# Kernel optimization log

Hardware: AMD Instinct MI355X
Metric: run time of the kernel (lower is better)

The kernel has to match this reference:

```python
import jax, jax.numpy as jnp
import numpy as np

N_LAYERS = 3


def setup_inputs() -> dict:
    key = jax.random.key(0)
    k1, k2, k3, k4 = jax.random.split(key, 4)
    n_users, n_items, d, E = 600000, 400000, 64, 2000000
    return {
        "user_emb": jax.random.normal(k1, (n_users, d), dtype=jnp.float32) * 0.1,
        "item_emb": jax.random.normal(k2, (n_items, d), dtype=jnp.float32) * 0.1,
        "user_ids": jax.random.randint(k3, (E,), 0, n_users, dtype=jnp.int64),
        "item_ids": jax.random.randint(k4, (E,), 0, n_items, dtype=jnp.int64),
    }


def reference(user_emb, item_emb, user_ids, item_ids):
    n_users = user_emb.shape[0]
    n_items = item_emb.shape[0]
    n_nodes = n_users + n_items
    # symmetrized bipartite edge list (user->item and item->user)
    rows = jnp.concatenate([user_ids, item_ids + n_users])
    cols = jnp.concatenate([item_ids + n_users, user_ids])
    # degree = row-sum of binary adjacency (duplicates counted, matching csr sum)
    deg = jax.ops.segment_sum(jnp.ones(rows.shape, dtype=user_emb.dtype), rows,
                              num_segments=n_nodes)
    d_inv_sqrt = (deg + 1e-8) ** -0.5
    vals = d_inv_sqrt[rows] * d_inv_sqrt[cols]  # per-edge normalized weight

    emb = jnp.concatenate([user_emb, item_emb], axis=0)  # [n_nodes, d]
    acc = emb
    x = emb
    for _ in range(N_LAYERS):
        x = jax.ops.segment_sum(vals[:, None] * x[cols], rows, num_segments=n_nodes)
        acc = acc + x
    final = acc / (N_LAYERS + 1)  # mean over stacked layer outputs
    return final[:n_users], final[n_users:]
```

## Files before the change

### kernel.cpp

```cpp
#include <hip/hip_runtime.h>


#define BLK 256
#define SCAN_CHUNK 2048
#define FILL_EPB 2048

typedef unsigned int u32;
typedef unsigned char u8;
typedef float __attribute__((ext_vector_type(4))) f32x4;

static inline int nblk(long long total) { return (int)((total + BLK - 1) / BLK); }

__device__ inline u32 pack_bf2(float lo, float hi) {
    u32 a = __float_as_uint(lo);
    u32 b = __float_as_uint(hi);
    a = a + 0x7fffu + ((a >> 16) & 1u);
    b = b + 0x7fffu + ((b >> 16) & 1u);
    return (a >> 16) | (b & 0xffff0000u);
}

__device__ inline void unpack_acc(uint4 w, float* a) {
    a[0] += __uint_as_float(w.x << 16);
    a[1] += __uint_as_float(w.x & 0xffff0000u);
    a[2] += __uint_as_float(w.y << 16);
    a[3] += __uint_as_float(w.y & 0xffff0000u);
    a[4] += __uint_as_float(w.z << 16);
    a[5] += __uint_as_float(w.z & 0xffff0000u);
    a[6] += __uint_as_float(w.w << 16);
    a[7] += __uint_as_float(w.w & 0xffff0000u);
}

__device__ inline void unpack8(uint4 w, float* a) {
    a[0] = __uint_as_float(w.x << 16);
    a[1] = __uint_as_float(w.x & 0xffff0000u);
    a[2] = __uint_as_float(w.y << 16);
    a[3] = __uint_as_float(w.y & 0xffff0000u);
    a[4] = __uint_as_float(w.z << 16);
    a[5] = __uint_as_float(w.z & 0xffff0000u);
    a[6] = __uint_as_float(w.w << 16);
    a[7] = __uint_as_float(w.w & 0xffff0000u);
}

__global__ void deg_rank_kernel(const int* __restrict__ uid,
                                const int* __restrict__ iid,
                                int E, int n_users,
                                u32* __restrict__ degw,
                                u32* __restrict__ rank2) {
    int t = blockIdx.x * blockDim.x + threadIdx.x;
    if (t < E) {
        u32 u  = (u32)uid[t];
        u32 iN = (u32)(n_users + iid[t]);
        u32 su = 8u * (u & 3u), si = 8u * (iN & 3u);
        u32 r0 = atomicAdd(&degw[u >> 2],  1u << su);
        u32 r1 = atomicAdd(&degw[iN >> 2], 1u << si);
        r0 = (r0 >> su) & 0xffu;
        r1 = (r1 >> si) & 0xffu;
        rank2[t] = r0 | (r1 << 16);
    }
}

__global__ void dinv_kernel(const u8* __restrict__ deg8,
                            float* __restrict__ dinv, int n_nodes) {
    int t = blockIdx.x * blockDim.x + threadIdx.x;
    if (t < n_nodes) dinv[t] = rsqrtf((float)deg8[t] + 1e-8f);
}

__global__ void scan1_kernel(const u8* __restrict__ deg8,
                             u32* __restrict__ rp, u32* __restrict__ bsum, int n) {
    __shared__ u32 ts[256];
    int tid = threadIdx.x;
    int base = blockIdx.x * SCAN_CHUNK + tid * 8;
    u32 v[8];
    u32 s = 0;
    #pragma unroll
    for (int i = 0; i < 8; ++i) {
        v[i] = (base + i < n) ? (u32)deg8[base + i] : 0u;
        s += v[i];
    }
    ts[tid] = s;
    __syncthreads();
    for (int off = 1; off < 256; off <<= 1) {
        u32 a = (tid >= off) ? ts[tid - off] : 0u;
        __syncthreads();
        ts[tid] += a;
        __syncthreads();
    }
    u32 run = (tid > 0) ? ts[tid - 1] : 0u;
    #pragma unroll
    for (int i = 0; i < 8; ++i) {
        run += v[i];
        if (base + i < n) rp[base + i + 1] = run;
    }
    if (tid == 255) bsum[blockIdx.x] = ts[255];
}

__global__ void scan2_kernel(u32* __restrict__ bsum, int nb) {
    __shared__ u32 s[1024];
    int tid = threadIdx.x;
    s[tid] = (tid < nb) ? bsum[tid] : 0u;
    __syncthreads();
    for (int off = 1; off < 1024; off <<= 1) {
        u32 a = (tid >= off) ? s[tid - off] : 0u;
        __syncthreads();
        s[tid] += a;
        __syncthreads();
    }
    if (tid < nb) bsum[tid] = (tid == 0) ? 0u : s[tid - 1];
}

__global__ void scan3_kernel(u32* __restrict__ rp,
                             const u32* __restrict__ bsum, int n) {
    int t = blockIdx.x * blockDim.x + threadIdx.x;
    if (t < n) rp[t + 1] += bsum[t / SCAN_CHUNK];
    if (t == 0) rp[0] = 0u;
}

__global__ void fill_sliced_kernel(const int* __restrict__ uid,
                                   const int* __restrict__ iid,
                                   const u32* __restrict__ rank2,
                                   const u32* __restrict__ rp,
                                   int E, int n_users, int shift,
                                   int* __restrict__ ci) {
    int slice = blockIdx.x & 7;
    int chunk = blockIdx.x >> 3;
    int e0   = chunk * FILL_EPB;
    int eend = min(E, e0 + FILL_EPB);
    for (int e = e0 + threadIdx.x; e < eend; e += BLK) {
        int u  = uid[e];
        int iN = n_users + iid[e];
        u32 rr = rank2[e];
        if ((u >> shift) == slice)  ci[rp[u]  + (rr & 0xffffu)] = iN;
        if ((iN >> shift) == slice) ci[rp[iN] + (rr >> 16)]     = u;
    }
}

__global__ void z0_full_kernel(const f32x4* __restrict__ uemb,
                               const f32x4* __restrict__ iemb,
                               const float* __restrict__ dinv,
                               uint4* __restrict__ z0,
                               int n_users, int n_nodes) {
    long long t = (long long)blockIdx.x * blockDim.x + threadIdx.x;
    if (t >= (long long)n_nodes * 8) return;
    int row = (int)(t >> 3);
    int j   = (int)(t & 7);
    const f32x4* src = (row < n_users)
                           ? uemb + (size_t)row * 16 + j * 2
                           : iemb + (size_t)(row - n_users) * 16 + j * 2;
    f32x4 p = __builtin_nontemporal_load(src);
    f32x4 q = __builtin_nontemporal_load(src + 1);
    float w = dinv[row];
    uint4 o;
    o.x = pack_bf2(w * p.x, w * p.y);
    o.y = pack_bf2(w * p.z, w * p.w);
    o.z = pack_bf2(w * q.x, w * q.y);
    o.w = pack_bf2(w * q.z, w * q.w);
    z0[(size_t)row * 8 + j] = o;
}

__global__ void spmm_mid64(const u32* __restrict__ rp,
                           const int* __restrict__ ci,
                           const float* __restrict__ dinv,
                           const uint4* __restrict__ src,
                           uint4* __restrict__ dst, int n_nodes) {
    long long t = (long long)blockIdx.x * blockDim.x + threadIdx.x;
    int row = (int)(t >> 3);
    if (row >= n_nodes) return;
    int j = (int)(t & 7);
    const uint4* sp = src + j;
    u32 k = rp[row], end = rp[row + 1];
    float a[8] = {0.f, 0.f, 0.f, 0.f, 0.f, 0.f, 0.f, 0.f};
    for (; k + 3 < end; k += 4) {
        int c0 = ci[k], c1 = ci[k + 1], c2 = ci[k + 2], c3 = ci[k + 3];
        uint4 w0 = sp[(size_t)c0 * 8];
        uint4 w1 = sp[(size_t)c1 * 8];
        uint4 w2 = sp[(size_t)c2 * 8];
        uint4 w3 = sp[(size_t)c3 * 8];
        unpack_acc(w0, a); unpack_acc(w1, a);
        unpack_acc(w2, a); unpack_acc(w3, a);
    }
    for (; k < end; ++k) {
        uint4 w0 = sp[(size_t)ci[k] * 8];
        unpack_acc(w0, a);
    }
    float dr = dinv[row];
    float s = dr * dr;
    uint4 o;
    o.x = pack_bf2(s * a[0], s * a[1]);
    o.y = pack_bf2(s * a[2], s * a[3]);
    o.z = pack_bf2(s * a[4], s * a[5]);
    o.w = pack_bf2(s * a[6], s * a[7]);
    dst[(size_t)row * 8 + j] = o;
}

__global__ void spmm_final64(const u32* __restrict__ rp,
                             const int* __restrict__ ci,
                             const float* __restrict__ dinv,
                             const uint4* __restrict__ z2,
                             const uint4* __restrict__ z1,
                             const uint4* __restrict__ z0,
                             f32x4* __restrict__ out, int n_nodes) {
    long long t = (long long)blockIdx.x * blockDim.x + threadIdx.x;
    int row = (int)(t >> 3);
    if (row >= n_nodes) return;
    int j = (int)(t & 7);
    const uint4* sp = z2 + j;
    u32 k = rp[row], end = rp[row + 1];
    float a[8] = {0.f, 0.f, 0.f, 0.f, 0.f, 0.f, 0.f, 0.f};
    for (; k + 3 < end; k += 4) {
        int c0 = ci[k], c1 = ci[k + 1], c2 = ci[k + 2], c3 = ci[k + 3];
        uint4 w0 = sp[(size_t)c0 * 8];
        uint4 w1 = sp[(size_t)c1 * 8];
        uint4 w2 = sp[(size_t)c2 * 8];
        uint4 w3 = sp[(size_t)c3 * 8];
        unpack_acc(w0, a); unpack_acc(w1, a);
        unpack_acc(w2, a); unpack_acc(w3, a);
    }
    for (; k < end; ++k) {
        uint4 w0 = sp[(size_t)ci[k] * 8];
        unpack_acc(w0, a);
    }
    float dr = dinv[row];
    float inv = 1.0f / dr;

    float v0[8], v1[8], v2[8];
    unpack8(z0[(size_t)row * 8 + j], v0);
    unpack8(z1[(size_t)row * 8 + j], v1);
    unpack8(z2[(size_t)row * 8 + j], v2);

    float r[8];
    #pragma unroll
    for (int i = 0; i < 8; ++i)
        r[i] = 0.25f * ((v0[i] + v1[i] + v2[i]) * inv + dr * a[i]);

    size_t ob = (size_t)row * 16 + j * 2;
    f32x4 lo = {r[0], r[1], r[2], r[3]};
    f32x4 hi = {r[4], r[5], r[6], r[7]};
    __builtin_nontemporal_store(lo, out + ob);
    __builtin_nontemporal_store(hi, out + ob + 1);
}

extern "C" void kernel_launch(void* const* d_in, const int* in_sizes, int n_in,
                              void* d_out, int out_size, void* d_ws, size_t ws_size,
                              hipStream_t stream) {
    const float* uemb = (const float*)d_in[0];
    const float* iemb = (const float*)d_in[1];
    const int*   uid  = (const int*)d_in[2];
    const int*   iid  = (const int*)d_in[3];

    const int d = 64;
    int n_users = in_sizes[0] / d;
    int n_items = in_sizes[1] / d;
    int E       = in_sizes[2];
    int n_nodes = n_users + n_items;
    long long nnz = 2LL * E;

    auto align256 = [](size_t x) { return (x + 255) & ~(size_t)255; };
    size_t deg_b  = align256((size_t)n_nodes + 4);
    size_t rp_b   = align256((size_t)(n_nodes + 1) * 4);
    size_t dinv_b = align256((size_t)n_nodes * 4);
    size_t ci_b   = align256((size_t)nnz * 4);
    size_t rk_b   = align256((size_t)E * 4);
    size_t bs_b   = align256(4096 * 4);
    size_t z_b    = align256((size_t)n_nodes * 128);

    char* p = (char*)d_ws;
    u32*   degw  = (u32*)p;    p += deg_b;
    u32*   rp    = (u32*)p;    p += rp_b;
    float* dinv  = (float*)p;  p += dinv_b;
    int*   ci    = (int*)p;    p += ci_b;
    u32*   rank2 = (u32*)p;    p += rk_b;
    u32*   bsum  = (u32*)p;    p += bs_b;
    uint4* z0    = (uint4*)p;  p += z_b;
    uint4* z1    = (uint4*)p;  p += z_b;
    uint4* z2    = (uint4*)p;

    int shift = 0;
    while (((n_nodes - 1) >> shift) >= 8) shift++;

    hipMemsetAsync(degw, 0, (size_t)n_nodes + 4, stream);
    deg_rank_kernel<<<nblk(E), BLK, 0, stream>>>(uid, iid, E, n_users, degw, rank2);
    dinv_kernel<<<nblk(n_nodes), BLK, 0, stream>>>((const u8*)degw, dinv, n_nodes);

    int nb = (n_nodes + SCAN_CHUNK - 1) / SCAN_CHUNK;
    scan1_kernel<<<nb, 256, 0, stream>>>((const u8*)degw, rp, bsum, n_nodes);
    scan2_kernel<<<1, 1024, 0, stream>>>(bsum, nb);
    scan3_kernel<<<nblk(n_nodes), BLK, 0, stream>>>(rp, bsum, n_nodes);

    int nchunks = (E + FILL_EPB - 1) / FILL_EPB;
    fill_sliced_kernel<<<nchunks * 8, BLK, 0, stream>>>(
        uid, iid, rank2, rp, E, n_users, shift, ci);

    long long nt = (long long)n_nodes * 8;
    z0_full_kernel<<<nblk(nt), BLK, 0, stream>>>(
        (const f32x4*)uemb, (const f32x4*)iemb, dinv, z0, n_users, n_nodes);
    spmm_mid64<<<nblk(nt), BLK, 0, stream>>>(rp, ci, dinv, z0, z1, n_nodes);
    spmm_mid64<<<nblk(nt), BLK, 0, stream>>>(rp, ci, dinv, z1, z2, n_nodes);
    spmm_final64<<<nblk(nt), BLK, 0, stream>>>(rp, ci, dinv, z2, z1, z0,
                                               (f32x4*)d_out, n_nodes);
}
```

Measured before the change: 712.0 us.

## Fuse embedding bf16 conversion into degree kernel and scale by dinv in first SpMM

The bf16 conversion of the input embeddings no longer depends on the degree normalization. It now runs in the same launch as the degree/rank atomics, using a block-index split, so it can overlap with that atomic-bound work. The first SpMM instead gathers dinv per neighbor and applies the source-side scaling on the fly. The final combine is adjusted because z0 is now unscaled. This removes one dependent kernel launch from the critical path but adds per-edge dinv gathers in the first propagation layer.

```diff
diff --git a/kernel.cpp b/kernel.cpp
--- a/kernel.cpp
+++ b/kernel.cpp
@@ -30,6 +30,17 @@
     a[7] += __uint_as_float(w.w & 0xffff0000u);
 }
 
+__device__ inline void unpack_acc_s(uint4 w, float s, float* a) {
+    a[0] += s * __uint_as_float(w.x << 16);
+    a[1] += s * __uint_as_float(w.x & 0xffff0000u);
+    a[2] += s * __uint_as_float(w.y << 16);
+    a[3] += s * __uint_as_float(w.y & 0xffff0000u);
+    a[4] += s * __uint_as_float(w.z << 16);
+    a[5] += s * __uint_as_float(w.z & 0xffff0000u);
+    a[6] += s * __uint_as_float(w.w << 16);
+    a[7] += s * __uint_as_float(w.w & 0xffff0000u);
+}
+
 __device__ inline void unpack8(uint4 w, float* a) {
     a[0] = __uint_as_float(w.x << 16);
     a[1] = __uint_as_float(w.x & 0xffff0000u);
@@ -41,21 +52,41 @@
     a[7] = __uint_as_float(w.w & 0xffff0000u);
 }
 
-__global__ void deg_rank_kernel(const int* __restrict__ uid,
-                                const int* __restrict__ iid,
-                                int E, int n_users,
-                                u32* __restrict__ degw,
-                                u32* __restrict__ rank2) {
-    int t = blockIdx.x * blockDim.x + threadIdx.x;
-    if (t < E) {
-        u32 u  = (u32)uid[t];
-        u32 iN = (u32)(n_users + iid[t]);
-        u32 su = 8u * (u & 3u), si = 8u * (iN & 3u);
-        u32 r0 = atomicAdd(&degw[u >> 2],  1u << su);
-        u32 r1 = atomicAdd(&degw[iN >> 2], 1u << si);
-        r0 = (r0 >> su) & 0xffu;
-        r1 = (r1 >> si) & 0xffu;
-        rank2[t] = r0 | (r1 << 16);
+__global__ void fused_deg_conv(const int* __restrict__ uid,
+                               const int* __restrict__ iid,
+                               int E, int n_users,
+                               u32* __restrict__ degw,
+                               u32* __restrict__ rank2,
+                               const f32x4* __restrict__ uemb,
+                               const f32x4* __restrict__ iemb,
+                               uint4* __restrict__ z0,
+                               int n_nodes, int nblk_deg) {
+    if ((int)blockIdx.x < nblk_deg) {
+        int t = blockIdx.x * BLK + threadIdx.x;
+        if (t < E) {
+            u32 u  = (u32)uid[t];
+            u32 iN = (u32)(n_users + iid[t]);
+            u32 su = 8u * (u & 3u), si = 8u * (iN & 3u);
+            u32 r0 = atomicAdd(&degw[u >> 2],  1u << su);
+            u32 r1 = atomicAdd(&degw[iN >> 2], 1u << si);
+            rank2[t] = ((r0 >> su) & 0xffu) | (((r1 >> si) & 0xffu) << 16);
+        }
+    } else {
+        long long t = (long long)(blockIdx.x - nblk_deg) * BLK + threadIdx.x;
+        if (t >= (long long)n_nodes * 8) return;
+        int row = (int)(t >> 3);
+        int j   = (int)(t & 7);
+        const f32x4* src = (row < n_users)
+                               ? uemb + (size_t)row * 16 + j * 2
+                               : iemb + (size_t)(row - n_users) * 16 + j * 2;
+        f32x4 p = __builtin_nontemporal_load(src);
+        f32x4 q = __builtin_nontemporal_load(src + 1);
+        uint4 o;
+        o.x = pack_bf2(p.x, p.y);
+        o.y = pack_bf2(p.z, p.w);
+        o.z = pack_bf2(q.x, q.y);
+        o.w = pack_bf2(q.z, q.w);
+        z0[(size_t)row * 8 + j] = o;
     }
 }
 
@@ -134,27 +165,41 @@
     }
 }
 
-__global__ void z0_full_kernel(const f32x4* __restrict__ uemb,
-                               const f32x4* __restrict__ iemb,
-                               const float* __restrict__ dinv,
-                               uint4* __restrict__ z0,
-                               int n_users, int n_nodes) {
+__global__ void spmm_first64(const u32* __restrict__ rp,
+                             const int* __restrict__ ci,
+                             const float* __restrict__ dinv,
+                             const uint4* __restrict__ z0p,
+                             uint4* __restrict__ dst, int n_nodes) {
     long long t = (long long)blockIdx.x * blockDim.x + threadIdx.x;
-    if (t >= (long long)n_nodes * 8) return;
     int row = (int)(t >> 3);
-    int j   = (int)(t & 7);
-    const f32x4* src = (row < n_users)
-                           ? uemb + (size_t)row * 16 + j * 2
-                           : iemb + (size_t)(row - n_users) * 16 + j * 2;
-    f32x4 p = __builtin_nontemporal_load(src);
-    f32x4 q = __builtin_nontemporal_load(src + 1);
-    float w = dinv[row];
+    if (row >= n_nodes) return;
+    int j = (int)(t & 7);
+    const uint4* sp = z0p + j;
+    u32 k = rp[row], end = rp[row + 1];
+    float a[8] = {0.f, 0.f, 0.f, 0.f, 0.f, 0.f, 0.f, 0.f};
+    for (; k + 3 < end; k += 4) {
+        int c0 = ci[k], c1 = ci[k + 1], c2 = ci[k + 2], c3 = ci[k + 3];
+        uint4 w0 = sp[(size_t)c0 * 8];
+        uint4 w1 = sp[(size_t)c1 * 8];
+        uint4 w2 = sp[(size_t)c2 * 8];
+        uint4 w3 = sp[(size_t)c3 * 8];
+        float d0 = dinv[c0], d1 = dinv[c1], d2 = dinv[c2], d3 = dinv[c3];
+        unpack_acc_s(w0, d0, a); unpack_acc_s(w1, d1, a);
+        unpack_acc_s(w2, d2, a); unpack_acc_s(w3, d3, a);
+    }
+    for (; k < end; ++k) {
+        int c0 = ci[k];
+        uint4 w0 = sp[(size_t)c0 * 8];
+        unpack_acc_s(w0, dinv[c0], a);
+    }
+    float dr = dinv[row];
+    float s = dr * dr;
     uint4 o;
-    o.x = pack_bf2(w * p.x, w * p.y);
-    o.y = pack_bf2(w * p.z, w * p.w);
-    o.z = pack_bf2(w * q.x, w * q.y);
-    o.w = pack_bf2(w * q.z, w * q.w);
-    z0[(size_t)row * 8 + j] = o;
+    o.x = pack_bf2(s * a[0], s * a[1]);
+    o.y = pack_bf2(s * a[2], s * a[3]);
+    o.z = pack_bf2(s * a[4], s * a[5]);
+    o.w = pack_bf2(s * a[6], s * a[7]);
+    dst[(size_t)row * 8 + j] = o;
 }
 
 __global__ void spmm_mid64(const u32* __restrict__ rp,
@@ -230,7 +275,7 @@
     float r[8];
     #pragma unroll
     for (int i = 0; i < 8; ++i)
-        r[i] = 0.25f * ((v0[i] + v1[i] + v2[i]) * inv + dr * a[i]);
+        r[i] = 0.25f * (v0[i] + (v1[i] + v2[i]) * inv + dr * a[i]);
 
     size_t ob = (size_t)row * 16 + j * 2;
     f32x4 lo = {r[0], r[1], r[2], r[3]};
@@ -278,7 +323,11 @@
     while (((n_nodes - 1) >> shift) >= 8) shift++;
 
     hipMemsetAsync(degw, 0, (size_t)n_nodes + 4, stream);
-    deg_rank_kernel<<<nblk(E), BLK, 0, stream>>>(uid, iid, E, n_users, degw, rank2);
+    int nblk_deg  = nblk(E);
+    int nblk_conv = nblk((long long)n_nodes * 8);
+    fused_deg_conv<<<nblk_deg + nblk_conv, BLK, 0, stream>>>(
+        uid, iid, E, n_users, degw, rank2,
+        (const f32x4*)uemb, (const f32x4*)iemb, z0, n_nodes, nblk_deg);
     dinv_kernel<<<nblk(n_nodes), BLK, 0, stream>>>((const u8*)degw, dinv, n_nodes);
 
     int nb = (n_nodes + SCAN_CHUNK - 1) / SCAN_CHUNK;
@@ -291,9 +340,7 @@
         uid, iid, rank2, rp, E, n_users, shift, ci);
 
     long long nt = (long long)n_nodes * 8;
-    z0_full_kernel<<<nblk(nt), BLK, 0, stream>>>(
-        (const f32x4*)uemb, (const f32x4*)iemb, dinv, z0, n_users, n_nodes);
-    spmm_mid64<<<nblk(nt), BLK, 0, stream>>>(rp, ci, dinv, z0, z1, n_nodes);
+    spmm_first64<<<nblk(nt), BLK, 0, stream>>>(rp, ci, dinv, z0, z1, n_nodes);
     spmm_mid64<<<nblk(nt), BLK, 0, stream>>>(rp, ci, dinv, z1, z2, n_nodes);
     spmm_final64<<<nblk(nt), BLK, 0, stream>>>(rp, ci, dinv, z2, z1, z0,
                                                (f32x4*)d_out, n_nodes);
```

Result: no change. 719.8 us (+1.1%).
